# Performance work log

Measured on AMD Instinct MI355X. Metric: run time of the kernel, lower is better.

## Reference

```python
import jax, jax.numpy as jnp
import numpy as np

N_NODES = 100000
N_EDGES = 1600000
NFEAT = 256
NHID = 128
NCLASS = 8


def setup_inputs() -> dict:
    key = jax.random.key(0)
    k1, k2, k3, k4, k5 = jax.random.split(key, 5)
    x = jax.random.normal(k1, (N_NODES, NFEAT), dtype=jnp.float32)
    edge_index = jax.random.randint(k2, (2, N_EDGES), 0, N_NODES, dtype=jnp.int64)
    # GCNConv weight (glorot) and bias
    s1 = float(np.sqrt(6.0 / (NFEAT + NHID)))
    W1 = jax.random.uniform(k3, (NFEAT, NHID), dtype=jnp.float32, minval=-s1, maxval=s1)
    b1 = jnp.zeros((NHID,), dtype=jnp.float32)
    # fc Linear (xavier uniform per weights_init, bias zero)
    s2 = float(np.sqrt(6.0 / (NHID + NCLASS)))
    Wfc = jax.random.uniform(k4, (NHID, NCLASS), dtype=jnp.float32, minval=-s2, maxval=s2)
    bfc = jnp.zeros((NCLASS,), dtype=jnp.float32)
    return {"x": x, "edge_index": edge_index, "W1": W1, "b1": b1, "Wfc": Wfc, "bfc": bfc}


def gcn_conv(x, src, dst, W, b, n_nodes):
    # PyG GCNConv: h = X W; out_i = sum_j norm_ij * h_j over A+I with sym norm
    h = x @ W  # [N, nhid]
    deg = jax.ops.segment_sum(jnp.ones_like(dst, dtype=h.dtype), dst, num_segments=n_nodes)
    dinv = jnp.where(deg > 0, jax.lax.rsqrt(deg), 0.0)  # deg^{-1/2}
    norm = dinv[src] * dinv[dst]  # [E+N]
    msg = h[src] * norm[:, None]  # gather + scale, [E+N, nhid]
    out = jax.ops.segment_sum(msg, dst, num_segments=n_nodes)
    return out + b


def reference(x, edge_index, W1, b1, Wfc, bfc):
    n = x.shape[0]
    loop = jnp.arange(n, dtype=edge_index.dtype)
    src = jnp.concatenate([edge_index[0], loop])  # add self-loops
    dst = jnp.concatenate([edge_index[1], loop])
    h = gcn_conv(x, src, dst, W1, b1, n)  # GCN_Body (no activation in forward)
    return h @ Wfc + bfc  # fc
```

## Files before the change

kernel.cpp:

```cpp
#include <hip/hip_runtime.h>
#include <hip/hip_bf16.h>

#define N_NODES 100000
#define N_EDGES 1600000
#define NFEAT 256
#define NHID 128
#define NCLASS 8

#define NBLK 512
#define BSH 8
#define BUCK 256
#define NBUCK ((N_NODES + BUCK - 1) / BUCK)
#define CAPE 6144

__global__ __launch_bounds__(256) void hist_kernel(const int* __restrict__ edst,
                                                   int* __restrict__ blockhist,
                                                   int chunk, int nE) {
    __shared__ int h[NBUCK];
    int tid = threadIdx.x;
    for (int i = tid; i < NBUCK; i += 256) h[i] = 0;
    __syncthreads();
    int e0 = blockIdx.x * chunk;
    int e1 = min(e0 + chunk, nE);
    for (int e = e0 + tid; e < e1; e += 256)
        atomicAdd(&h[edst[e] >> BSH], 1);
    __syncthreads();
    for (int i = tid; i < NBUCK; i += 256)
        blockhist[(long)blockIdx.x * NBUCK + i] = h[i];
}

__global__ __launch_bounds__(256) void scanblk_kernel(const int* __restrict__ blockhist,
                                                      int* __restrict__ blockbase,
                                                      int* __restrict__ bucket_total) {
    __shared__ int ss[256];
    int b = blockIdx.x, tid = threadIdx.x;
    int v0 = blockhist[(long)tid * NBUCK + b];
    int v1 = blockhist[(long)(tid + 256) * NBUCK + b];
    int t = v0 + v1;
    ss[tid] = t; __syncthreads();
    for (int o = 1; o < 256; o <<= 1) {
        int u = (tid >= o) ? ss[tid - o] : 0;
        __syncthreads(); ss[tid] += u; __syncthreads();
    }
    int ex = ss[tid] - t;
    blockbase[(long)tid * NBUCK + b] = ex;
    blockbase[(long)(tid + 256) * NBUCK + b] = ex + v0;
    if (tid == 255) bucket_total[b] = ss[255];
}

__global__ __launch_bounds__(512) void mid_kernel(const int* __restrict__ bucket_total,
                                                  int* __restrict__ bucket_base,
                                                  const float* __restrict__ W1,
                                                  const float* __restrict__ b1,
                                                  const float* __restrict__ Wfc,
                                                  const float* __restrict__ bfc,
                                                  float* __restrict__ WcT,
                                                  float* __restrict__ cvec) {
    int tid = threadIdx.x;
    if (blockIdx.x == 0) {
        __shared__ int ss[512];
        int v = (tid < NBUCK) ? bucket_total[tid] : 0;
        ss[tid] = v; __syncthreads();
        for (int o = 1; o < 512; o <<= 1) {
            int u = (tid >= o) ? ss[tid - o] : 0;
            __syncthreads(); ss[tid] += u; __syncthreads();
        }
        if (tid < NBUCK) bucket_base[tid] = ss[tid] - v;
        if (tid == NBUCK - 1) bucket_base[NBUCK] = ss[tid];
    } else {
        __shared__ float wfs[NHID * NCLASS];
        __shared__ float bs[NHID];
        for (int i = tid; i < NHID * NCLASS; i += 512) wfs[i] = Wfc[i];
        if (tid < NHID) bs[tid] = b1[tid];
        __syncthreads();
        if (tid < NFEAT) {
            float acc[NCLASS] = {};
            for (int h = 0; h < NHID; h++) {
                float w = W1[tid * NHID + h];
                #pragma unroll
                for (int c = 0; c < NCLASS; c++) acc[c] += w * wfs[h * NCLASS + c];
            }
            #pragma unroll
            for (int c = 0; c < NCLASS; c++) WcT[c * NFEAT + tid] = acc[c];
        }
        if (tid < NCLASS) {
            float a = bfc[tid];
            for (int h = 0; h < NHID; h++) a += bs[h] * wfs[h * NCLASS + tid];
            cvec[tid] = a;
        }
    }
}

__global__ __launch_bounds__(256) void scat_kernel(const int* __restrict__ esrc,
                                                   const int* __restrict__ edst,
                                                   const int* __restrict__ blockbase,
                                                   const int* __restrict__ bucket_base,
                                                   int* __restrict__ ebufP,
                                                   int chunk, int nE) {
    __shared__ int cur[NBUCK];
    int tid = threadIdx.x;
    for (int i = tid; i < NBUCK; i += 256)
        cur[i] = bucket_base[i] + blockbase[(long)blockIdx.x * NBUCK + i];
    __syncthreads();
    int e0 = blockIdx.x * chunk;
    int e1 = min(e0 + chunk, nE);
    for (int e = e0 + tid; e < e1; e += 256) {
        int s = esrc[e];
        int d = edst[e];
        int pos = atomicAdd(&cur[d >> BSH], 1);
        ebufP[pos] = (s << BSH) | (d & (BUCK - 1));
    }
}

__global__ __launch_bounds__(256) void deg_dinv_kernel(const int* __restrict__ ebufP,
                                                       const int* __restrict__ bucket_base,
                                                       float* __restrict__ dinv) {
    __shared__ int cnt[BUCK];
    int b = blockIdx.x, tid = threadIdx.x;
    cnt[tid] = 0;
    __syncthreads();
    int base = bucket_base[b], end = bucket_base[b + 1];
    for (int e = base + tid; e < end; e += 256)
        atomicAdd(&cnt[ebufP[e] & (BUCK - 1)], 1);
    __syncthreads();
    int node = (b << BSH) + tid;
    if (node < N_NODES) dinv[node] = rsqrtf((float)(cnt[tid] + 1));
}

__global__ __launch_bounds__(256) void z_kernel(const float* __restrict__ X,
                                                const float* __restrict__ WcT,
                                                const float* __restrict__ dinv,
                                                float* __restrict__ Zs, int n) {
    __shared__ float4 wlds[NCLASS * 64];
    int tid = threadIdx.x;
    #pragma unroll
    for (int i = tid; i < NCLASS * 64; i += 256)
        wlds[i] = ((const float4*)WcT)[i];
    __syncthreads();

    const int lane = tid & 63;
    const int sub  = lane & 7;
    const int rsub = lane >> 3;
    const int wid  = (blockIdx.x * 256 + tid) >> 6;
    const int nw   = (gridDim.x * 256) >> 6;
    const int ngroups = (n + 7) >> 3;

    for (int g = wid; g < ngroups; g += nw) {
        int row = g * 8 + rsub;
        bool ok = row < n;
        int r = ok ? row : (n - 1);
        const float4* xr = (const float4*)(X + (long)r * NFEAT);
        float4 xv[8];
        #pragma unroll
        for (int k = 0; k < 8; k++) xv[k] = xr[sub + 8 * k];

        float res = 0.f;
        #pragma unroll
        for (int c = 0; c < NCLASS; c++) {
            float s = 0.f;
            #pragma unroll
            for (int k = 0; k < 8; k++) {
                float4 w = wlds[c * 64 + sub + 8 * k];
                s += xv[k].x * w.x + xv[k].y * w.y + xv[k].z * w.z + xv[k].w * w.w;
            }
            s += __shfl_xor(s, 1);
            s += __shfl_xor(s, 2);
            s += __shfl_xor(s, 4);
            if (sub == c) res = s;
        }
        if (ok) Zs[(long)row * NCLASS + sub] = res * dinv[row];
    }
}

__global__ __launch_bounds__(512) void sort_gather_kernel(
        const float* __restrict__ Zs,
        const int* __restrict__ ebufP,
        const int* __restrict__ bucket_base,
        const float* __restrict__ dinv,
        const float* __restrict__ cvec,
        float* __restrict__ out, int n) {
    __shared__ int cnt[BUCK];
    __shared__ int off[BUCK + 1];
    __shared__ int ss[BUCK];
    __shared__ int sorted[CAPE];
    int b = blockIdx.x, tid = threadIdx.x;
    int base = bucket_base[b], end = bucket_base[b + 1];
    int total = end - base;
    const float4* Zs4 = (const float4*)Zs;
    float4 c0v = ((const float4*)cvec)[0];
    float4 c1v = ((const float4*)cvec)[1];

    if (total <= CAPE) {
        if (tid < BUCK) cnt[tid] = 0;
        __syncthreads();
        for (int e = base + tid; e < end; e += 512)
            atomicAdd(&cnt[ebufP[e] & (BUCK - 1)], 1);
        __syncthreads();

        int t = (tid < BUCK) ? cnt[tid] : 0;
        if (tid < BUCK) ss[tid] = t;
        __syncthreads();
        for (int o = 1; o < BUCK; o <<= 1) {
            int u = 0;
            if (tid < BUCK && tid >= o) u = ss[tid - o];
            __syncthreads();
            if (tid < BUCK) ss[tid] += u;
            __syncthreads();
        }
        if (tid < BUCK) {
            off[tid] = ss[tid] - t;
            cnt[tid] = ss[tid] - t;
            if (tid == BUCK - 1) off[BUCK] = ss[tid];
        }
        __syncthreads();

        for (int e = base + tid; e < end; e += 512) {
            int p = ebufP[e];
            int slot = atomicAdd(&cnt[p & (BUCK - 1)], 1);
            sorted[slot] = p >> BSH;
        }
        __syncthreads();

        int li = tid >> 1;
        int h  = tid & 1;
        int node = (b << BSH) + li;
        if (node < n) {
            int k0 = off[li], k1 = off[li + 1];
            float4 a = Zs4[node * 2 + h];
            int k = k0;
            for (; k + 1 < k1; k += 2) {
                int s0 = sorted[k], s1 = sorted[k + 1];
                float4 z0 = Zs4[s0 * 2 + h];
                float4 z1 = Zs4[s1 * 2 + h];
                a.x += z0.x + z1.x; a.y += z0.y + z1.y;
                a.z += z0.z + z1.z; a.w += z0.w + z1.w;
            }
            if (k < k1) {
                float4 z = Zs4[sorted[k] * 2 + h];
                a.x += z.x; a.y += z.y; a.z += z.z; a.w += z.w;
            }
            float dd = dinv[node];
            float4 cv = h ? c1v : c0v;
            float4 o;
            o.x = a.x * dd + cv.x; o.y = a.y * dd + cv.y;
            o.z = a.z * dd + cv.z; o.w = a.w * dd + cv.w;
            ((float4*)out)[node * 2 + h] = o;
        }
    } else {
        float* acc = (float*)sorted;
        for (int i = tid; i < NCLASS * BUCK; i += 512) acc[i] = 0.f;
        __syncthreads();
        for (int e = base + tid; e < end; e += 512) {
            int p = ebufP[e];
            int src = p >> BSH;
            int li = p & (BUCK - 1);
            float4 z0 = Zs4[src * 2];
            float4 z1 = Zs4[src * 2 + 1];
            atomicAdd(&acc[0 * BUCK + li], z0.x);
            atomicAdd(&acc[1 * BUCK + li], z0.y);
            atomicAdd(&acc[2 * BUCK + li], z0.z);
            atomicAdd(&acc[3 * BUCK + li], z0.w);
            atomicAdd(&acc[4 * BUCK + li], z1.x);
            atomicAdd(&acc[5 * BUCK + li], z1.y);
            atomicAdd(&acc[6 * BUCK + li], z1.z);
            atomicAdd(&acc[7 * BUCK + li], z1.w);
        }
        __syncthreads();
        if (tid < BUCK) {
            int node = (b << BSH) + tid;
            if (node < n) {
                float4 s0 = Zs4[node * 2];
                float4 s1 = Zs4[node * 2 + 1];
                float dd = dinv[node];
                float4 o0, o1;
                o0.x = (s0.x + acc[0 * BUCK + tid]) * dd + c0v.x;
                o0.y = (s0.y + acc[1 * BUCK + tid]) * dd + c0v.y;
                o0.z = (s0.z + acc[2 * BUCK + tid]) * dd + c0v.z;
                o0.w = (s0.w + acc[3 * BUCK + tid]) * dd + c0v.w;
                o1.x = (s1.x + acc[4 * BUCK + tid]) * dd + c1v.x;
                o1.y = (s1.y + acc[5 * BUCK + tid]) * dd + c1v.y;
                o1.z = (s1.z + acc[6 * BUCK + tid]) * dd + c1v.z;
                o1.w = (s1.w + acc[7 * BUCK + tid]) * dd + c1v.w;
                ((float4*)out)[node * 2]     = o0;
                ((float4*)out)[node * 2 + 1] = o1;
            }
        }
    }
}

extern "C" void kernel_launch(void* const* d_in, const int* in_sizes, int n_in,
                              void* d_out, int out_size, void* d_ws, size_t ws_size,
                              hipStream_t stream) {
    const float* x    = (const float*)d_in[0];
    const int*   eidx = (const int*)d_in[1];
    const float* W1   = (const float*)d_in[2];
    const float* b1   = (const float*)d_in[3];
    const float* Wfc  = (const float*)d_in[4];
    const float* bfc  = (const float*)d_in[5];
    float* out = (float*)d_out;

    const int N = N_NODES;
    const int E = in_sizes[1] / 2;
    const int chunk = (E + NBLK - 1) / NBLK;

    const int* esrc = eidx;
    const int* edst = eidx + E;

    float* Zs    = (float*)d_ws;
    float* dinv  = Zs + (long)8 * N;
    float* cvec  = dinv + N;
    float* WcT   = cvec + 8;
    int*   btot  = (int*)(WcT + NCLASS * NFEAT);
    int*   bbase = btot + NBUCK + 1;
    int*   bhist = bbase + NBUCK + 3;
    int*   bbas2 = bhist + (long)NBLK * NBUCK;
    int*   ebufP = bbas2 + (long)NBLK * NBUCK;

    hist_kernel<<<NBLK, 256, 0, stream>>>(edst, bhist, chunk, E);
    scanblk_kernel<<<NBUCK, 256, 0, stream>>>(bhist, bbas2, btot);
    mid_kernel<<<2, 512, 0, stream>>>(btot, bbase, W1, b1, Wfc, bfc, WcT, cvec);
    scat_kernel<<<NBLK, 256, 0, stream>>>(esrc, edst, bbas2, bbase, ebufP, chunk, E);
    deg_dinv_kernel<<<NBUCK, 256, 0, stream>>>(ebufP, bbase, dinv);
    z_kernel<<<1563, 256, 0, stream>>>(x, WcT, dinv, Zs, N);
    sort_gather_kernel<<<NBUCK, 512, 0, stream>>>(Zs, ebufP, bbase, dinv, cvec, out, N);
}
```

Baseline: 243.0 us.

## Vectorize edge loads with int4, double histogram blocks, recompute dinv in gather

```diff
diff --git a/kernel.cpp b/kernel.cpp
--- a/kernel.cpp
+++ b/kernel.cpp
@@ -7,7 +7,7 @@
 #define NHID 128
 #define NCLASS 8
 
-#define NBLK 512
+#define NBLK 1024
 #define BSH 8
 #define BUCK 256
 #define NBUCK ((N_NODES + BUCK - 1) / BUCK)
@@ -22,8 +22,16 @@
     __syncthreads();
     int e0 = blockIdx.x * chunk;
     int e1 = min(e0 + chunk, nE);
-    for (int e = e0 + tid; e < e1; e += 256)
-        atomicAdd(&h[edst[e] >> BSH], 1);
+    for (int e = e0 + tid * 4; e + 3 < e1; e += 1024) {
+        int4 d = *(const int4*)&edst[e];
+        atomicAdd(&h[d.x >> BSH], 1);
+        atomicAdd(&h[d.y >> BSH], 1);
+        atomicAdd(&h[d.z >> BSH], 1);
+        atomicAdd(&h[d.w >> BSH], 1);
+    }
+    int full = e0 + ((e1 - e0) & ~3);
+    int et = full + tid;
+    if (et < e1) atomicAdd(&h[edst[et] >> BSH], 1);
     __syncthreads();
     for (int i = tid; i < NBUCK; i += 256)
         blockhist[(long)blockIdx.x * NBUCK + i] = h[i];
@@ -34,17 +42,21 @@
                                                       int* __restrict__ bucket_total) {
     __shared__ int ss[256];
     int b = blockIdx.x, tid = threadIdx.x;
-    int v0 = blockhist[(long)tid * NBUCK + b];
-    int v1 = blockhist[(long)(tid + 256) * NBUCK + b];
-    int t = v0 + v1;
+    int v0 = blockhist[(long)(tid * 4 + 0) * NBUCK + b];
+    int v1 = blockhist[(long)(tid * 4 + 1) * NBUCK + b];
+    int v2 = blockhist[(long)(tid * 4 + 2) * NBUCK + b];
+    int v3 = blockhist[(long)(tid * 4 + 3) * NBUCK + b];
+    int t = v0 + v1 + v2 + v3;
     ss[tid] = t; __syncthreads();
     for (int o = 1; o < 256; o <<= 1) {
         int u = (tid >= o) ? ss[tid - o] : 0;
         __syncthreads(); ss[tid] += u; __syncthreads();
     }
     int ex = ss[tid] - t;
-    blockbase[(long)tid * NBUCK + b] = ex;
-    blockbase[(long)(tid + 256) * NBUCK + b] = ex + v0;
+    blockbase[(long)(tid * 4 + 0) * NBUCK + b] = ex;
+    blockbase[(long)(tid * 4 + 1) * NBUCK + b] = ex + v0;
+    blockbase[(long)(tid * 4 + 2) * NBUCK + b] = ex + v0 + v1;
+    blockbase[(long)(tid * 4 + 3) * NBUCK + b] = ex + v0 + v1 + v2;
     if (tid == 255) bucket_total[b] = ss[255];
 }
 
@@ -104,27 +116,52 @@
     __syncthreads();
     int e0 = blockIdx.x * chunk;
     int e1 = min(e0 + chunk, nE);
-    for (int e = e0 + tid; e < e1; e += 256) {
-        int s = esrc[e];
-        int d = edst[e];
+    for (int e = e0 + tid * 4; e + 3 < e1; e += 1024) {
+        int4 s = *(const int4*)&esrc[e];
+        int4 d = *(const int4*)&edst[e];
+        int p0 = atomicAdd(&cur[d.x >> BSH], 1);
+        int p1 = atomicAdd(&cur[d.y >> BSH], 1);
+        int p2 = atomicAdd(&cur[d.z >> BSH], 1);
+        int p3 = atomicAdd(&cur[d.w >> BSH], 1);
+        ebufP[p0] = (s.x << BSH) | (d.x & (BUCK - 1));
+        ebufP[p1] = (s.y << BSH) | (d.y & (BUCK - 1));
+        ebufP[p2] = (s.z << BSH) | (d.z & (BUCK - 1));
+        ebufP[p3] = (s.w << BSH) | (d.w & (BUCK - 1));
+    }
+    int full = e0 + ((e1 - e0) & ~3);
+    int et = full + tid;
+    if (et < e1) {
+        int s = esrc[et], d = edst[et];
         int pos = atomicAdd(&cur[d >> BSH], 1);
         ebufP[pos] = (s << BSH) | (d & (BUCK - 1));
     }
 }
 
-__global__ __launch_bounds__(256) void deg_dinv_kernel(const int* __restrict__ ebufP,
+__global__ __launch_bounds__(512) void deg_dinv_kernel(const int* __restrict__ ebufP,
                                                        const int* __restrict__ bucket_base,
                                                        float* __restrict__ dinv) {
     __shared__ int cnt[BUCK];
     int b = blockIdx.x, tid = threadIdx.x;
-    cnt[tid] = 0;
+    if (tid < BUCK) cnt[tid] = 0;
     __syncthreads();
     int base = bucket_base[b], end = bucket_base[b + 1];
-    for (int e = base + tid; e < end; e += 256)
-        atomicAdd(&cnt[ebufP[e] & (BUCK - 1)], 1);
-    __syncthreads();
-    int node = (b << BSH) + tid;
-    if (node < N_NODES) dinv[node] = rsqrtf((float)(cnt[tid] + 1));
+    int a0 = min((base + 3) & ~3, end);
+    if (base + tid < a0) atomicAdd(&cnt[ebufP[base + tid] & (BUCK - 1)], 1);
+    for (int e = a0 + tid * 4; e + 3 < end; e += 2048) {
+        int4 p = *(const int4*)&ebufP[e];
+        atomicAdd(&cnt[p.x & (BUCK - 1)], 1);
+        atomicAdd(&cnt[p.y & (BUCK - 1)], 1);
+        atomicAdd(&cnt[p.z & (BUCK - 1)], 1);
+        atomicAdd(&cnt[p.w & (BUCK - 1)], 1);
+    }
+    int full = a0 + ((end - a0) & ~3);
+    int et = full + tid;
+    if (et < end) atomicAdd(&cnt[ebufP[et] & (BUCK - 1)], 1);
+    __syncthreads();
+    if (tid < BUCK) {
+        int node = (b << BSH) + tid;
+        if (node < N_NODES) dinv[node] = rsqrtf((float)(cnt[tid] + 1));
+    }
 }
 
 __global__ __launch_bounds__(256) void z_kernel(const float* __restrict__ X,
@@ -176,7 +213,6 @@
         const float* __restrict__ Zs,
         const int* __restrict__ ebufP,
         const int* __restrict__ bucket_base,
-        const float* __restrict__ dinv,
         const float* __restrict__ cvec,
         float* __restrict__ out, int n) {
     __shared__ int cnt[BUCK];
@@ -193,8 +229,17 @@
     if (total <= CAPE) {
         if (tid < BUCK) cnt[tid] = 0;
         __syncthreads();
-        for (int e = base + tid; e < end; e += 512)
-            atomicAdd(&cnt[ebufP[e] & (BUCK - 1)], 1);
+        int a0 = min((base + 3) & ~3, end);
+        if (base + tid < a0) atomicAdd(&cnt[ebufP[base + tid] & (BUCK - 1)], 1);
+        for (int e = a0 + tid * 4; e + 3 < end; e += 2048) {
+            int4 p = *(const int4*)&ebufP[e];
+            atomicAdd(&cnt[p.x & (BUCK - 1)], 1);
+            atomicAdd(&cnt[p.y & (BUCK - 1)], 1);
+            atomicAdd(&cnt[p.z & (BUCK - 1)], 1);
+            atomicAdd(&cnt[p.w & (BUCK - 1)], 1);
+        }
+        int full = a0 + ((end - a0) & ~3);
+        if (full + tid < end) atomicAdd(&cnt[ebufP[full + tid] & (BUCK - 1)], 1);
         __syncthreads();
 
         int t = (tid < BUCK) ? cnt[tid] : 0;
@@ -214,8 +259,24 @@
         }
         __syncthreads();
 
-        for (int e = base + tid; e < end; e += 512) {
-            int p = ebufP[e];
+        if (base + tid < a0) {
+            int p = ebufP[base + tid];
+            int slot = atomicAdd(&cnt[p & (BUCK - 1)], 1);
+            sorted[slot] = p >> BSH;
+        }
+        for (int e = a0 + tid * 4; e + 3 < end; e += 2048) {
+            int4 p = *(const int4*)&ebufP[e];
+            int s0 = atomicAdd(&cnt[p.x & (BUCK - 1)], 1);
+            int s1 = atomicAdd(&cnt[p.y & (BUCK - 1)], 1);
+            int s2 = atomicAdd(&cnt[p.z & (BUCK - 1)], 1);
+            int s3 = atomicAdd(&cnt[p.w & (BUCK - 1)], 1);
+            sorted[s0] = p.x >> BSH;
+            sorted[s1] = p.y >> BSH;
+            sorted[s2] = p.z >> BSH;
+            sorted[s3] = p.w >> BSH;
+        }
+        if (full + tid < end) {
+            int p = ebufP[full + tid];
             int slot = atomicAdd(&cnt[p & (BUCK - 1)], 1);
             sorted[slot] = p >> BSH;
         }
@@ -239,7 +300,7 @@
                 float4 z = Zs4[sorted[k] * 2 + h];
                 a.x += z.x; a.y += z.y; a.z += z.z; a.w += z.w;
             }
-            float dd = dinv[node];
+            float dd = rsqrtf((float)(k1 - k0 + 1));
             float4 cv = h ? c1v : c0v;
             float4 o;
             o.x = a.x * dd + cv.x; o.y = a.y * dd + cv.y;
@@ -248,12 +309,15 @@
         }
     } else {
         float* acc = (float*)sorted;
+        __shared__ int dcount[BUCK];
+        if (tid < BUCK) dcount[tid] = 0;
         for (int i = tid; i < NCLASS * BUCK; i += 512) acc[i] = 0.f;
         __syncthreads();
         for (int e = base + tid; e < end; e += 512) {
             int p = ebufP[e];
             int src = p >> BSH;
             int li = p & (BUCK - 1);
+            atomicAdd(&dcount[li], 1);
             float4 z0 = Zs4[src * 2];
             float4 z1 = Zs4[src * 2 + 1];
             atomicAdd(&acc[0 * BUCK + li], z0.x);
@@ -271,7 +335,7 @@
             if (node < n) {
                 float4 s0 = Zs4[node * 2];
                 float4 s1 = Zs4[node * 2 + 1];
-                float dd = dinv[node];
+                float dd = rsqrtf((float)(dcount[tid] + 1));
                 float4 o0, o1;
                 o0.x = (s0.x + acc[0 * BUCK + tid]) * dd + c0v.x;
                 o0.y = (s0.y + acc[1 * BUCK + tid]) * dd + c0v.y;
@@ -301,7 +365,7 @@
 
     const int N = N_NODES;
     const int E = in_sizes[1] / 2;
-    const int chunk = (E + NBLK - 1) / NBLK;
+    const int chunk = (((E + NBLK - 1) / NBLK) + 3) & ~3;
 
     const int* esrc = eidx;
     const int* edst = eidx + E;
@@ -312,15 +376,17 @@
     float* WcT   = cvec + 8;
     int*   btot  = (int*)(WcT + NCLASS * NFEAT);
     int*   bbase = btot + NBUCK + 1;
-    int*   bhist = bbase + NBUCK + 3;
+    int*   bhist = bbase + NBUCK + 4;
     int*   bbas2 = bhist + (long)NBLK * NBUCK;
-    int*   ebufP = bbas2 + (long)NBLK * NBUCK;
+    size_t ofs = (size_t)(bbas2 + (long)NBLK * NBUCK - (int*)d_ws);
+    ofs = (ofs + 3) & ~(size_t)3;
+    int*   ebufP = (int*)d_ws + ofs;
 
     hist_kernel<<<NBLK, 256, 0, stream>>>(edst, bhist, chunk, E);
     scanblk_kernel<<<NBUCK, 256, 0, stream>>>(bhist, bbas2, btot);
     mid_kernel<<<2, 512, 0, stream>>>(btot, bbase, W1, b1, Wfc, bfc, WcT, cvec);
     scat_kernel<<<NBLK, 256, 0, stream>>>(esrc, edst, bbas2, bbase, ebufP, chunk, E);
-    deg_dinv_kernel<<<NBUCK, 256, 0, stream>>>(ebufP, bbase, dinv);
+    deg_dinv_kernel<<<NBUCK, 512, 0, stream>>>(ebufP, bbase, dinv);
     z_kernel<<<1563, 256, 0, stream>>>(x, WcT, dinv, Zs, N);
-    sort_gather_kernel<<<NBUCK, 512, 0, stream>>>(Zs, ebufP, bbase, dinv, cvec, out, N);
-}
+    sort_gather_kernel<<<NBUCK, 512, 0, stream>>>(Zs, ebufP, bbase, cvec, out, N);
+}
```

New measurement: 238.9 us. Within noise of the previous version (-1.7%).
